# Optimization experiments

Measured on AMD Instinct MI355X. Metric: run time of the kernel, lower is better.

The kernel has to match this reference:

```python
import jax, jax.numpy as jnp
import numpy as np

B, L, HID, NH, NB = 8, 1024, 512, 8, 8
HD = HID // NH


def setup_inputs() -> dict:
    key = jax.random.key(0)
    ks = jax.random.split(key, 12)
    s = 1.0 / np.sqrt(HID)
    x = jax.random.normal(ks[0], (B, L, HID), dtype=jnp.float32)
    time_bucket_matrix = jax.random.randint(ks[1], (B, L, L), 0, NB, dtype=jnp.int32)
    causal_mask = jnp.triu(jnp.ones((L, L), dtype=bool), k=1)  # True = masked (future)
    lens = jax.random.randint(ks[2], (B,), (7 * L) // 8, L + 1)
    padding_mask = jnp.arange(L)[None, :] >= lens[:, None]  # True = pad
    return {
        "x": x,
        "time_bucket_matrix": time_bucket_matrix,
        "causal_mask": causal_mask,
        "padding_mask": padding_mask,
        "Wq": jax.random.uniform(ks[3], (HID, HID), jnp.float32, -s, s),
        "bq": jnp.zeros((HID,), jnp.float32),
        "Wk": jax.random.uniform(ks[4], (HID, HID), jnp.float32, -s, s),
        "bk": jnp.zeros((HID,), jnp.float32),
        "Wv": jax.random.uniform(ks[5], (HID, HID), jnp.float32, -s, s),
        "bv": jnp.zeros((HID,), jnp.float32),
        "Wo": jax.random.uniform(ks[6], (HID, HID), jnp.float32, -s, s),
        "bo": jnp.zeros((HID,), jnp.float32),
        "time_emb": jax.random.normal(ks[7], (NB, NH), dtype=jnp.float32),
    }


def reference(x, time_bucket_matrix, causal_mask, padding_mask,
              Wq, bq, Wk, bk, Wv, bv, Wo, bo, time_emb):
    Bb, Ll, H = x.shape
    def heads(t):
        return t.reshape(Bb, Ll, NH, HD).transpose(0, 2, 1, 3)  # [B,NH,L,HD]
    q = heads(x @ Wq.T + bq)
    k = heads(x @ Wk.T + bk)
    v = heads(x @ Wv.T + bv)
    scores = jnp.einsum("bhqd,bhkd->bhqk", q, k) / jnp.sqrt(jnp.float32(HD))
    # per-(i,j) time-bucket bias: [B,L,L] -> [B,L,L,NH] -> [B,NH,L,L]
    t_bias = time_emb[time_bucket_matrix].transpose(0, 3, 1, 2)
    scores = scores + t_bias
    scores = jnp.where(causal_mask[None, None, :, :], -1e9, scores)
    scores = jnp.where(padding_mask[:, None, None, :], -1e9, scores)  # key pad
    w = jax.nn.softmax(scores, axis=-1)
    w = jnp.where(padding_mask[:, None, :, None], 0.0, w)  # query pad
    out = jnp.einsum("bhqk,bhkd->bhqd", w, v).transpose(0, 2, 1, 3).reshape(Bb, Ll, H)
    return out @ Wo.T + bo
```

## Files before the change

kernel.cpp:

```cpp
#include <hip/hip_runtime.h>
#include <hip/hip_bf16.h>
#include <cstdint>

#define L_SEQ 1024
#define HID_DIM 512
#define N_HEADS 8
#define HEAD_DIM 64
#define BATCH 8

typedef __attribute__((ext_vector_type(8))) short bf16x8;
typedef __attribute__((ext_vector_type(4))) float f32x4;

__device__ __forceinline__ ushort f2bf(float v) {
  __hip_bfloat16 hb = __float2bfloat16(v);
  return *(ushort*)&hb;
}

__global__ __launch_bounds__(256)
void prep_convert(const float* __restrict__ x, const float* __restrict__ Wq,
                  const float* __restrict__ Wk, const float* __restrict__ Wv,
                  const float* __restrict__ Wo, ushort* __restrict__ dst) {
  const size_t gid = (size_t)blockIdx.x * 256 + threadIdx.x;
  const size_t e = gid * 8;
  const float* src;
  size_t loc;
  if (e < 4194304) {
    src = x; loc = e;
  } else {
    const size_t r = e - 4194304;
    const int wsel = (int)(r >> 18);
    loc = r & 262143;
    src = (wsel == 0) ? Wq : (wsel == 1) ? Wk : (wsel == 2) ? Wv : Wo;
  }
  float4 v0 = *(const float4*)(src + loc);
  float4 v1 = *(const float4*)(src + loc + 4);
  ushort u[8];
  u[0] = f2bf(v0.x); u[1] = f2bf(v0.y); u[2] = f2bf(v0.z); u[3] = f2bf(v0.w);
  u[4] = f2bf(v1.x); u[5] = f2bf(v1.y); u[6] = f2bf(v1.z); u[7] = f2bf(v1.w);
  *(uint4*)(dst + e) = *(uint4*)u;
}

__global__ __launch_bounds__(256)
void lens_kernel(const uint8_t* __restrict__ pm, int* __restrict__ lens) {
  __shared__ int flag;
  __shared__ int part[256];
  const int b = blockIdx.x, tid = threadIdx.x;
  if (tid == 0) flag = 0;
  __syncthreads();
  const unsigned* pw = (const unsigned*)pm;
  unsigned any = 0;
  for (int i = tid; i < 2048; i += 256) any |= (pw[i] > 1u);
  if (any) flag = 1;
  __syncthreads();
  int c = 0;
  if (flag) {
    unsigned v = pw[b * 256 + tid];
    c = (int)((v & 0xFFu) == 0) + (int)(((v >> 8) & 0xFFu) == 0) +
        (int)(((v >> 16) & 0xFFu) == 0) + (int)(((v >> 24) & 0xFFu) == 0);
  } else {
    const int* pi = (const int*)pm;
    c = (int)(pi[b * 1024 + tid * 4 + 0] == 0) + (int)(pi[b * 1024 + tid * 4 + 1] == 0) +
        (int)(pi[b * 1024 + tid * 4 + 2] == 0) + (int)(pi[b * 1024 + tid * 4 + 3] == 0);
  }
  part[tid] = c;
  __syncthreads();
  for (int s = 128; s > 0; s >>= 1) {
    if (tid < s) part[tid] += part[tid + s];
    __syncthreads();
  }
  if (tid == 0) lens[b] = part[0];
}

__global__ __launch_bounds__(256, 3)
void qkv_lds(const ushort* __restrict__ xb, const ushort* __restrict__ wqb,
             const ushort* __restrict__ wkb, const ushort* __restrict__ wvb,
             const float* __restrict__ bq, const float* __restrict__ bk,
             const float* __restrict__ bv, ushort* __restrict__ qb,
             ushort* __restrict__ kb, ushort* __restrict__ vT) {
  __shared__ char lds[2][20480];
  const int tid = threadIdx.x;
  const int w = tid >> 6, lane = tid & 63;
  const int l15 = lane & 15, g = lane >> 4;
  const int z = blockIdx.z;
  const ushort* A = (z == 2) ? wvb : xb;
  const ushort* B = (z == 0) ? wqb : (z == 1) ? wkb : xb;
  const float* bias = (z == 0) ? bq : (z == 1) ? bk : bv;
  const int M0 = ((z == 2) ? blockIdx.y : blockIdx.x) * 128;
  const int N0 = ((z == 2) ? blockIdx.x : blockIdx.y) * 128;

  const int sr = tid >> 2, sc = tid & 3;
  const ushort* Ag = A + (size_t)(M0 + sr) * 512 + sc * 8;
  const ushort* Bg = B + (size_t)(N0 + sr) * 512 + sc * 8;
  const int wro = sr * 80 + sc * 16;
  uint4 sa0, sa1, sb0, sb1;

#define QSTAGE_LOAD(kc_)                                      \
  sa0 = *(const uint4*)(Ag + (kc_) * 32);                     \
  sa1 = *(const uint4*)(Ag + (size_t)64 * 512 + (kc_) * 32);  \
  sb0 = *(const uint4*)(Bg + (kc_) * 32);                     \
  sb1 = *(const uint4*)(Bg + (size_t)64 * 512 + (kc_) * 32);
#define QSTAGE_WRITE(buf)                                     \
  *(uint4*)&(buf)[wro] = sa0;                                 \
  *(uint4*)&(buf)[wro + 64 * 80] = sa1;                       \
  *(uint4*)&(buf)[10240 + wro] = sb0;                         \
  *(uint4*)&(buf)[10240 + wro + 64 * 80] = sb1;

  const int wm = w >> 1, wn = w & 1;
  const int aro = (wm * 64 + l15) * 80 + g * 16;
  const int bro = 10240 + (wn * 64 + l15) * 80 + g * 16;

  f32x4 acc[4][4];
#pragma unroll
  for (int i = 0; i < 4; ++i)
#pragma unroll
    for (int j = 0; j < 4; ++j) acc[i][j] = (f32x4){0.f, 0.f, 0.f, 0.f};

  QSTAGE_LOAD(0);
  QSTAGE_WRITE(lds[0]);
  __syncthreads();
  int cur = 0;
#pragma unroll 1
  for (int kc = 0; kc < 16; ++kc) {
    if (kc + 1 < 16) { QSTAGE_LOAD(kc + 1); }
    bf16x8 av[4], bv[4];
#pragma unroll
    for (int t = 0; t < 4; ++t) {
      av[t] = *(const bf16x8*)&lds[cur][aro + t * 1280];
      bv[t] = *(const bf16x8*)&lds[cur][bro + t * 1280];
    }
    __builtin_amdgcn_s_setprio(1);
#pragma unroll
    for (int i = 0; i < 4; ++i)
#pragma unroll
      for (int j = 0; j < 4; ++j)
        acc[i][j] = __builtin_amdgcn_mfma_f32_16x16x32_bf16(av[i], bv[j], acc[i][j], 0, 0, 0);
    __builtin_amdgcn_s_setprio(0);
    if (kc + 1 < 16) { QSTAGE_WRITE(lds[cur ^ 1]); }
    __syncthreads();
    cur ^= 1;
  }
#undef QSTAGE_LOAD
#undef QSTAGE_WRITE

  const int M0w = M0 + wm * 64, N0w = N0 + wn * 64;
  if (z < 2) {
    ushort* out = (z == 0) ? qb : kb;
    float bn[4];
#pragma unroll
    for (int nt = 0; nt < 4; ++nt) bn[nt] = bias[N0w + nt * 16 + l15];
#pragma unroll
    for (int mt = 0; mt < 4; ++mt)
#pragma unroll
      for (int nt = 0; nt < 4; ++nt)
#pragma unroll
        for (int r = 0; r < 4; ++r) {
          const int m = M0w + mt * 16 + 4 * g + r;
          const int n = N0w + nt * 16 + l15;
          out[(size_t)m * 512 + n] = f2bf(acc[mt][nt][r] + bn[nt]);
        }
  } else {
#pragma unroll
    for (int mt = 0; mt < 4; ++mt)
#pragma unroll
      for (int r = 0; r < 4; ++r) {
        const int m = M0w + mt * 16 + 4 * g + r;
        const float bm = bias[m];
#pragma unroll
        for (int nt = 0; nt < 4; ++nt) {
          const int tok = N0w + nt * 16 + l15;
          const size_t off = ((size_t)((tok >> 10) * 512 + m)) * 1024 + (tok & 1023);
          vT[off] = f2bf(acc[mt][nt][r] + bm);
        }
      }
  }
}

__global__ __launch_bounds__(256, 3)
void out_lds(const ushort* __restrict__ A, const ushort* __restrict__ B,
             const float* __restrict__ bias, float* __restrict__ out) {
  __shared__ char lds[2][15360];
  const int tid = threadIdx.x;
  const int w = tid >> 6, lane = tid & 63;
  const int l15 = lane & 15, g = lane >> 4;
  const int M0 = blockIdx.x * 64, N0 = blockIdx.y * 128;

  const int sr = tid >> 2, sc = tid & 3;
  const ushort* Ag = A + (size_t)(M0 + sr) * 512 + sc * 8;
  const ushort* Bg = B + (size_t)(N0 + sr) * 512 + sc * 8;
  const int wro = sr * 80 + sc * 16;
  uint4 sa0, sb0, sb1;

#define OSTAGE_LOAD(kc_)                                      \
  sa0 = *(const uint4*)(Ag + (kc_) * 32);                     \
  sb0 = *(const uint4*)(Bg + (kc_) * 32);                     \
  sb1 = *(const uint4*)(Bg + (size_t)64 * 512 + (kc_) * 32);
#define OSTAGE_WRITE(buf)                                     \
  *(uint4*)&(buf)[wro] = sa0;                                 \
  *(uint4*)&(buf)[5120 + wro] = sb0;                          \
  *(uint4*)&(buf)[5120 + wro + 64 * 80] = sb1;

  const int wm = w >> 1, wn = w & 1;
  const int aro = (wm * 32 + l15) * 80 + g * 16;
  const int bro = 5120 + (wn * 64 + l15) * 80 + g * 16;

  f32x4 acc[2][4];
#pragma unroll
  for (int i = 0; i < 2; ++i)
#pragma unroll
    for (int j = 0; j < 4; ++j) acc[i][j] = (f32x4){0.f, 0.f, 0.f, 0.f};

  OSTAGE_LOAD(0);
  OSTAGE_WRITE(lds[0]);
  __syncthreads();
  int cur = 0;
#pragma unroll 1
  for (int kc = 0; kc < 16; ++kc) {
    if (kc + 1 < 16) { OSTAGE_LOAD(kc + 1); }
    bf16x8 av[2], bv[4];
#pragma unroll
    for (int t = 0; t < 2; ++t) av[t] = *(const bf16x8*)&lds[cur][aro + t * 1280];
#pragma unroll
    for (int t = 0; t < 4; ++t) bv[t] = *(const bf16x8*)&lds[cur][bro + t * 1280];
    __builtin_amdgcn_s_setprio(1);
#pragma unroll
    for (int i = 0; i < 2; ++i)
#pragma unroll
      for (int j = 0; j < 4; ++j)
        acc[i][j] = __builtin_amdgcn_mfma_f32_16x16x32_bf16(av[i], bv[j], acc[i][j], 0, 0, 0);
    __builtin_amdgcn_s_setprio(0);
    if (kc + 1 < 16) { OSTAGE_WRITE(lds[cur ^ 1]); }
    __syncthreads();
    cur ^= 1;
  }
#undef OSTAGE_LOAD
#undef OSTAGE_WRITE

  const int M0w = M0 + wm * 32, N0w = N0 + wn * 64;
  float bn[4];
#pragma unroll
  for (int nt = 0; nt < 4; ++nt) bn[nt] = bias[N0w + nt * 16 + l15];
#pragma unroll
  for (int mt = 0; mt < 2; ++mt)
#pragma unroll
    for (int nt = 0; nt < 4; ++nt)
#pragma unroll
      for (int r = 0; r < 4; ++r) {
        const int m = M0w + mt * 16 + 4 * g + r;
        const int n = N0w + nt * 16 + l15;
        out[(size_t)m * 512 + n] = acc[mt][nt][r] + bn[nt];
      }
}

__global__ __launch_bounds__(256, 2)
void attn_mfma(const ushort* __restrict__ qb, const ushort* __restrict__ kb,
               const ushort* __restrict__ vT, const int* __restrict__ tbm,
               const float* __restrict__ temb, const int* __restrict__ lens,
               ushort* __restrict__ ab) {
  __shared__ char kv[2][16384];
  __shared__ char pbuf[4][2048];
  const int tid = threadIdx.x;
  const int w = tid >> 6;
  const int lane = tid & 63;
  const int l15 = lane & 15, g = lane >> 4;
  const int b = blockIdx.x, h = blockIdx.y, p = blockIdx.z;
  const int len = lens[b];
  const int GB = 15 - p;
  const int qbaseA = p * 64 + 16 * w;
  const int qbaseB = GB * 64 + 16 * w;

  const float te_src = temb[(lane & 7) * N_HEADS + h] * 1.44269504f;

  const int r0 = tid >> 3, c0 = tid & 7;
  const size_t kgrow = (size_t)(b * L_SEQ) * HID_DIM + h * HEAD_DIM + c0 * 8;
  const size_t vgrow = (size_t)((b * 8 + h) * 64 + r0) * L_SEQ + c0 * 8;
  const int so0 = (tid * 16) ^ ((r0 & 7) << 4);
  const int so1 = so0 + 4096;
  uint4 skA, skB, svA, svB;

#define STAGE_LOAD(kc_)                                                      \
  skA = *(const uint4*)(kb + kgrow + (size_t)((kc_) + r0) * HID_DIM);        \
  skB = *(const uint4*)(kb + kgrow + (size_t)((kc_) + r0 + 32) * HID_DIM);   \
  svA = *(const uint4*)(vT + vgrow + (kc_));                                 \
  svB = *(const uint4*)(vT + vgrow + 32 * L_SEQ + (kc_));

#define STAGE_WRITE(dst)                                                     \
  *(uint4*)&(dst)[so0] = skA;                                                \
  *(uint4*)&(dst)[so1] = skB;                                                \
  *(uint4*)&(dst)[8192 + so0] = svA;                                         \
  *(uint4*)&(dst)[8192 + so1] = svB;

  bf16x8 qfA[2], qfB[2];
  {
    const ushort* qr = qb + (size_t)(b * L_SEQ + qbaseA + l15) * HID_DIM + h * HEAD_DIM + 8 * g;
    qfA[0] = *(const bf16x8*)(qr);
    qfA[1] = *(const bf16x8*)(qr + 32);
    qr = qb + (size_t)(b * L_SEQ + qbaseB + l15) * HID_DIM + h * HEAD_DIM + 8 * g;
    qfB[0] = *(const bf16x8*)(qr);
    qfB[1] = *(const bf16x8*)(qr + 32);
  }

  f32x4 OA[4], OB[4];
#pragma unroll
  for (int ct = 0; ct < 4; ++ct) {
    OA[ct] = (f32x4){0.f, 0.f, 0.f, 0.f};
    OB[ct] = (f32x4){0.f, 0.f, 0.f, 0.f};
  }
  float ssA[4] = {0.f, 0.f, 0.f, 0.f}, ssB[4] = {0.f, 0.f, 0.f, 0.f};
  bf16x8 kf[4][2], vf[2][4];
  int tbA_[4][4], tbB_[4][4];

  const int lenc = (len - 1) >> 6;
  const int nchB = (GB * 64 < len) ? ((GB < lenc ? GB : lenc) + 1) : 0;
  const int NCH = (p + 1 > nchB) ? (p + 1) : nchB;

#define LOAD_TB(dst, qbaseT, kc_)                                            \
  {                                                                          \
    const int* tb_p = tbm + (size_t)(b * L_SEQ + (qbaseT)) * L_SEQ + (kc_);  \
    _Pragma("unroll") for (int kt = 0; kt < 4; ++kt)                         \
      _Pragma("unroll") for (int r = 0; r < 4; ++r)                          \
        dst[kt][r] = tb_p[(4 * g + r) * L_SEQ + 16 * kt + l15];              \
  }

#define LOAD_KV_FRAGS(kvb)                                                   \
  _Pragma("unroll") for (int kt = 0; kt < 4; ++kt)                           \
    _Pragma("unroll") for (int db = 0; db < 2; ++db) {                       \
      const int off = ((2048 * kt + 128 * l15 + 16 * (g + 4 * db)) ^ ((l15 & 7) << 4)); \
      kf[kt][db] = *(const bf16x8*)&(kvb)[off];                              \
    }                                                                        \
  _Pragma("unroll") for (int kblk = 0; kblk < 2; ++kblk)                     \
    _Pragma("unroll") for (int ct = 0; ct < 4; ++ct) {                       \
      const int off = 8192 + ((2048 * ct + 128 * l15 + 16 * (4 * kblk + g)) ^ ((l15 & 7) << 4)); \
      vf[kblk][ct] = *(const bf16x8*)&(kvb)[off];                            \
    }

#define COMPUTE_TILE(qfv, Ov, ssumv, tbv, qbaseT, kc_)                       \
  {                                                                          \
    f32x4 s[4];                                                              \
    __builtin_amdgcn_s_setprio(1);                                           \
    _Pragma("unroll") for (int kt = 0; kt < 4; ++kt) {                       \
      s[kt] = (f32x4){0.f, 0.f, 0.f, 0.f};                                   \
      s[kt] = __builtin_amdgcn_mfma_f32_16x16x32_bf16(qfv[0], kf[kt][0], s[kt], 0, 0, 0); \
      s[kt] = __builtin_amdgcn_mfma_f32_16x16x32_bf16(qfv[1], kf[kt][1], s[kt], 0, 0, 0); \
    }                                                                        \
    __builtin_amdgcn_s_setprio(0);                                           \
    _Pragma("unroll") for (int kt = 0; kt < 4; ++kt) {                       \
      const int kg = (kc_) + 16 * kt + l15;                                  \
      _Pragma("unroll") for (int r = 0; r < 4; ++r) {                        \
        const int lr = 4 * g + r;                                            \
        const int qg = (qbaseT) + lr;                                        \
        const float te2 = __int_as_float(                                    \
            __builtin_amdgcn_ds_bpermute(tbv[kt][r] << 2, __float_as_int(te_src))); \
        float pp = exp2f(fmaf(s[kt][r], 0.18033688f, te2));                  \
        pp = (kg <= qg && qg < len) ? pp : 0.0f;                             \
        const ushort pbits = f2bf(pp);                                       \
        ssumv[r] += __bfloat162float(*(const __hip_bfloat16*)&pbits);        \
        const int off = ((lr * 128 + (16 * kt + l15) * 2) ^ ((lr & 7) << 4)); \
        *(ushort*)&pbuf[w][off] = pbits;                                     \
      }                                                                      \
    }                                                                        \
    _Pragma("unroll") for (int kblk = 0; kblk < 2; ++kblk) {                 \
      const int off = ((l15 * 128 + kblk * 64 + 16 * g) ^ ((l15 & 7) << 4)); \
      const bf16x8 pf = *(const bf16x8*)(&pbuf[w][off]);                     \
      __builtin_amdgcn_s_setprio(1);                                         \
      _Pragma("unroll") for (int ct = 0; ct < 4; ++ct)                       \
        Ov[ct] = __builtin_amdgcn_mfma_f32_16x16x32_bf16(pf, vf[kblk][ct], Ov[ct], 0, 0, 0); \
      __builtin_amdgcn_s_setprio(0);                                         \
    }                                                                        \
  }

  STAGE_LOAD(0);
  STAGE_WRITE(kv[0]);
  __syncthreads();

  int cur = 0;
  for (int c = 0; c < NCH; ++c) {
    const int kc = c * 64;
    const bool doB = (c < nchB);
    const bool doA = (c <= p);
    if (doB) LOAD_TB(tbB_, qbaseB, kc);
    if (doA) LOAD_TB(tbA_, qbaseA, kc);
    if (c + 1 < NCH) { STAGE_LOAD(kc + 64); }
    LOAD_KV_FRAGS(kv[cur]);
    if (doB) COMPUTE_TILE(qfB, OB, ssB, tbB_, qbaseB, kc);
    if (doA) COMPUTE_TILE(qfA, OA, ssA, tbA_, qbaseA, kc);
    if (c + 1 < NCH) { STAGE_WRITE(kv[cur ^ 1]); }
    __syncthreads();
    cur ^= 1;
  }

#define EPILOGUE(Ov, ssumv, qbaseT)                                          \
  {                                                                          \
    _Pragma("unroll") for (int m = 1; m <= 8; m <<= 1)                       \
      _Pragma("unroll") for (int r = 0; r < 4; ++r)                          \
        ssumv[r] += __shfl_xor(ssumv[r], m, 64);                             \
    _Pragma("unroll") for (int ct = 0; ct < 4; ++ct)                         \
      _Pragma("unroll") for (int r = 0; r < 4; ++r) {                        \
        const int qg = (qbaseT) + 4 * g + r;                                 \
        const float inv = (qg < len) ? 1.0f / ssumv[r] : 0.0f;               \
        ab[(size_t)(b * L_SEQ + qg) * HID_DIM + h * HEAD_DIM + 16 * ct + l15] = \
            f2bf(Ov[ct][r] * inv);                                           \
      }                                                                      \
  }

  EPILOGUE(OA, ssA, qbaseA);
  EPILOGUE(OB, ssB, qbaseB);
}

extern "C" void kernel_launch(void* const* d_in, const int* in_sizes, int n_in,
                              void* d_out, int out_size, void* d_ws, size_t ws_size,
                              hipStream_t stream) {
  const float* x    = (const float*)d_in[0];
  const int*   tbm  = (const int*)d_in[1];
  const uint8_t* pm = (const uint8_t*)d_in[3];
  const float* Wq = (const float*)d_in[4];
  const float* bq = (const float*)d_in[5];
  const float* Wk = (const float*)d_in[6];
  const float* bk = (const float*)d_in[7];
  const float* Wv = (const float*)d_in[8];
  const float* bv = (const float*)d_in[9];
  const float* Wo = (const float*)d_in[10];
  const float* bo = (const float*)d_in[11];
  const float* temb = (const float*)d_in[12];
  float* out = (float*)d_out;

  const size_t NTOK = (size_t)BATCH * L_SEQ * HID_DIM;
  const size_t NW = 262144;
  ushort* ab  = (ushort*)d_ws;
  ushort* xb  = ab + NTOK;
  ushort* wqb = xb + NTOK;
  ushort* wkb = wqb + NW;
  ushort* wvb = wkb + NW;
  ushort* wob = wvb + NW;
  ushort* qb  = wob + NW;
  ushort* kb  = qb + NTOK;
  ushort* vT  = kb + NTOK;
  int* lens   = (int*)(vT + NTOK);

  prep_convert<<<2560, 256, 0, stream>>>(x, Wq, Wk, Wv, Wo, xb);
  lens_kernel<<<8, 256, 0, stream>>>(pm, lens);
  qkv_lds<<<dim3(64, 4, 3), 256, 0, stream>>>(xb, wqb, wkb, wvb, bq, bk, bv, qb, kb, vT);
  attn_mfma<<<dim3(8, 8, 8), 256, 0, stream>>>(qb, kb, vT, tbm, temb, lens, ab);
  out_lds<<<dim3(128, 4), 256, 0, stream>>>(ab, wob, bo, out);
}
```

Before: 84.97 us.

## Split paired causal query tiles into separate blocks with higher occupancy

```diff
diff --git a/kernel.cpp b/kernel.cpp
--- a/kernel.cpp
+++ b/kernel.cpp
@@ -251,7 +251,7 @@
       }
 }
 
-__global__ __launch_bounds__(256, 2)
+__global__ __launch_bounds__(256, 4)
 void attn_mfma(const ushort* __restrict__ qb, const ushort* __restrict__ kb,
                const ushort* __restrict__ vT, const int* __restrict__ tbm,
                const float* __restrict__ temb, const int* __restrict__ lens,
@@ -262,11 +262,10 @@
   const int w = tid >> 6;
   const int lane = tid & 63;
   const int l15 = lane & 15, g = lane >> 4;
-  const int b = blockIdx.x, h = blockIdx.y, p = blockIdx.z;
+  const int b = blockIdx.x, h = blockIdx.y;
+  const int qg = 15 - blockIdx.z;
   const int len = lens[b];
-  const int GB = 15 - p;
-  const int qbaseA = p * 64 + 16 * w;
-  const int qbaseB = GB * 64 + 16 * w;
+  const int qbase = qg * 64 + 16 * w;
 
   const float te_src = temb[(lane & 7) * N_HEADS + h] * 1.44269504f;
 
@@ -289,121 +288,116 @@
   *(uint4*)&(dst)[8192 + so0] = svA;                                         \
   *(uint4*)&(dst)[8192 + so1] = svB;
 
-  bf16x8 qfA[2], qfB[2];
+  bf16x8 qf[2];
   {
-    const ushort* qr = qb + (size_t)(b * L_SEQ + qbaseA + l15) * HID_DIM + h * HEAD_DIM + 8 * g;
-    qfA[0] = *(const bf16x8*)(qr);
-    qfA[1] = *(const bf16x8*)(qr + 32);
-    qr = qb + (size_t)(b * L_SEQ + qbaseB + l15) * HID_DIM + h * HEAD_DIM + 8 * g;
-    qfB[0] = *(const bf16x8*)(qr);
-    qfB[1] = *(const bf16x8*)(qr + 32);
-  }
-
-  f32x4 OA[4], OB[4];
-#pragma unroll
-  for (int ct = 0; ct < 4; ++ct) {
-    OA[ct] = (f32x4){0.f, 0.f, 0.f, 0.f};
-    OB[ct] = (f32x4){0.f, 0.f, 0.f, 0.f};
-  }
-  float ssA[4] = {0.f, 0.f, 0.f, 0.f}, ssB[4] = {0.f, 0.f, 0.f, 0.f};
-  bf16x8 kf[4][2], vf[2][4];
-  int tbA_[4][4], tbB_[4][4];
+    const ushort* qr = qb + (size_t)(b * L_SEQ + qbase + l15) * HID_DIM + h * HEAD_DIM + 8 * g;
+    qf[0] = *(const bf16x8*)(qr);
+    qf[1] = *(const bf16x8*)(qr + 32);
+  }
+
+  f32x4 O[4];
+#pragma unroll
+  for (int ct = 0; ct < 4; ++ct) O[ct] = (f32x4){0.f, 0.f, 0.f, 0.f};
+  float ssum[4] = {0.f, 0.f, 0.f, 0.f};
+  int tb_[4][4];
 
   const int lenc = (len - 1) >> 6;
-  const int nchB = (GB * 64 < len) ? ((GB < lenc ? GB : lenc) + 1) : 0;
-  const int NCH = (p + 1 > nchB) ? (p + 1) : nchB;
-
-#define LOAD_TB(dst, qbaseT, kc_)                                            \
-  {                                                                          \
-    const int* tb_p = tbm + (size_t)(b * L_SEQ + (qbaseT)) * L_SEQ + (kc_);  \
-    _Pragma("unroll") for (int kt = 0; kt < 4; ++kt)                         \
-      _Pragma("unroll") for (int r = 0; r < 4; ++r)                          \
-        dst[kt][r] = tb_p[(4 * g + r) * L_SEQ + 16 * kt + l15];              \
-  }
-
-#define LOAD_KV_FRAGS(kvb)                                                   \
-  _Pragma("unroll") for (int kt = 0; kt < 4; ++kt)                           \
-    _Pragma("unroll") for (int db = 0; db < 2; ++db) {                       \
-      const int off = ((2048 * kt + 128 * l15 + 16 * (g + 4 * db)) ^ ((l15 & 7) << 4)); \
-      kf[kt][db] = *(const bf16x8*)&(kvb)[off];                              \
-    }                                                                        \
-  _Pragma("unroll") for (int kblk = 0; kblk < 2; ++kblk)                     \
-    _Pragma("unroll") for (int ct = 0; ct < 4; ++ct) {                       \
-      const int off = 8192 + ((2048 * ct + 128 * l15 + 16 * (4 * kblk + g)) ^ ((l15 & 7) << 4)); \
-      vf[kblk][ct] = *(const bf16x8*)&(kvb)[off];                            \
+  const int nch = (qg * 64 < len) ? ((qg < lenc ? qg : lenc) + 1) : 0;
+  const int* tbq = tbm + (size_t)(b * L_SEQ + qbase) * L_SEQ;
+
+  if (nch > 0) {
+    STAGE_LOAD(0);
+    STAGE_WRITE(kv[0]);
+  }
+  __syncthreads();
+
+  int cur = 0;
+#pragma unroll 1
+  for (int c = 0; c < nch; ++c) {
+    const int kc = c * 64;
+#pragma unroll
+    for (int kt = 0; kt < 4; ++kt)
+#pragma unroll
+      for (int r = 0; r < 4; ++r)
+        tb_[kt][r] = tbq[(size_t)(4 * g + r) * L_SEQ + kc + 16 * kt + l15];
+    if (c + 1 < nch) { STAGE_LOAD(kc + 64); }
+
+    bf16x8 kf[4][2];
+#pragma unroll
+    for (int kt = 0; kt < 4; ++kt)
+#pragma unroll
+      for (int db = 0; db < 2; ++db) {
+        const int off = ((2048 * kt + 128 * l15 + 16 * (g + 4 * db)) ^ ((l15 & 7) << 4));
+        kf[kt][db] = *(const bf16x8*)&kv[cur][off];
+      }
+    f32x4 s[4];
+    __builtin_amdgcn_s_setprio(1);
+#pragma unroll
+    for (int kt = 0; kt < 4; ++kt) {
+      s[kt] = (f32x4){0.f, 0.f, 0.f, 0.f};
+      s[kt] = __builtin_amdgcn_mfma_f32_16x16x32_bf16(qf[0], kf[kt][0], s[kt], 0, 0, 0);
+      s[kt] = __builtin_amdgcn_mfma_f32_16x16x32_bf16(qf[1], kf[kt][1], s[kt], 0, 0, 0);
     }
-
-#define COMPUTE_TILE(qfv, Ov, ssumv, tbv, qbaseT, kc_)                       \
-  {                                                                          \
-    f32x4 s[4];                                                              \
-    __builtin_amdgcn_s_setprio(1);                                           \
-    _Pragma("unroll") for (int kt = 0; kt < 4; ++kt) {                       \
-      s[kt] = (f32x4){0.f, 0.f, 0.f, 0.f};                                   \
-      s[kt] = __builtin_amdgcn_mfma_f32_16x16x32_bf16(qfv[0], kf[kt][0], s[kt], 0, 0, 0); \
-      s[kt] = __builtin_amdgcn_mfma_f32_16x16x32_bf16(qfv[1], kf[kt][1], s[kt], 0, 0, 0); \
-    }                                                                        \
-    __builtin_amdgcn_s_setprio(0);                                           \
-    _Pragma("unroll") for (int kt = 0; kt < 4; ++kt) {                       \
-      const int kg = (kc_) + 16 * kt + l15;                                  \
-      _Pragma("unroll") for (int r = 0; r < 4; ++r) {                        \
-        const int lr = 4 * g + r;                                            \
-        const int qg = (qbaseT) + lr;                                        \
-        const float te2 = __int_as_float(                                    \
-            __builtin_amdgcn_ds_bpermute(tbv[kt][r] << 2, __float_as_int(te_src))); \
-        float pp = exp2f(fmaf(s[kt][r], 0.18033688f, te2));                  \
-        pp = (kg <= qg && qg < len) ? pp : 0.0f;                             \
-        const ushort pbits = f2bf(pp);                                       \
-        ssumv[r] += __bfloat162float(*(const __hip_bfloat16*)&pbits);        \
-        const int off = ((lr * 128 + (16 * kt + l15) * 2) ^ ((lr & 7) << 4)); \
-        *(ushort*)&pbuf[w][off] = pbits;                                     \
-      }                                                                      \
-    }                                                                        \
-    _Pragma("unroll") for (int kblk = 0; kblk < 2; ++kblk) {                 \
-      const int off = ((l15 * 128 + kblk * 64 + 16 * g) ^ ((l15 & 7) << 4)); \
-      const bf16x8 pf = *(const bf16x8*)(&pbuf[w][off]);                     \
-      __builtin_amdgcn_s_setprio(1);                                         \
-      _Pragma("unroll") for (int ct = 0; ct < 4; ++ct)                       \
-        Ov[ct] = __builtin_amdgcn_mfma_f32_16x16x32_bf16(pf, vf[kblk][ct], Ov[ct], 0, 0, 0); \
-      __builtin_amdgcn_s_setprio(0);                                         \
-    }                                                                        \
-  }
-
-  STAGE_LOAD(0);
-  STAGE_WRITE(kv[0]);
-  __syncthreads();
-
-  int cur = 0;
-  for (int c = 0; c < NCH; ++c) {
-    const int kc = c * 64;
-    const bool doB = (c < nchB);
-    const bool doA = (c <= p);
-    if (doB) LOAD_TB(tbB_, qbaseB, kc);
-    if (doA) LOAD_TB(tbA_, qbaseA, kc);
-    if (c + 1 < NCH) { STAGE_LOAD(kc + 64); }
-    LOAD_KV_FRAGS(kv[cur]);
-    if (doB) COMPUTE_TILE(qfB, OB, ssB, tbB_, qbaseB, kc);
-    if (doA) COMPUTE_TILE(qfA, OA, ssA, tbA_, qbaseA, kc);
-    if (c + 1 < NCH) { STAGE_WRITE(kv[cur ^ 1]); }
+    __builtin_amdgcn_s_setprio(0);
+
+    bf16x8 vf[2][4];
+#pragma unroll
+    for (int kblk = 0; kblk < 2; ++kblk)
+#pragma unroll
+      for (int ct = 0; ct < 4; ++ct) {
+        const int off = 8192 + ((2048 * ct + 128 * l15 + 16 * (4 * kblk + g)) ^ ((l15 & 7) << 4));
+        vf[kblk][ct] = *(const bf16x8*)&kv[cur][off];
+      }
+
+#pragma unroll
+    for (int kt = 0; kt < 4; ++kt) {
+      const int kg = kc + 16 * kt + l15;
+#pragma unroll
+      for (int r = 0; r < 4; ++r) {
+        const int lr = 4 * g + r;
+        const int qgr = qbase + lr;
+        const float te2 = __int_as_float(
+            __builtin_amdgcn_ds_bpermute(tb_[kt][r] << 2, __float_as_int(te_src)));
+        float pp = exp2f(fmaf(s[kt][r], 0.18033688f, te2));
+        pp = (kg <= qgr && qgr < len) ? pp : 0.0f;
+        ssum[r] += pp;
+        const int off = ((lr * 128 + (16 * kt + l15) * 2) ^ ((lr & 7) << 4));
+        *(ushort*)&pbuf[w][off] = f2bf(pp);
+      }
+    }
+
+#pragma unroll
+    for (int kblk = 0; kblk < 2; ++kblk) {
+      const int off = ((l15 * 128 + kblk * 64 + 16 * g) ^ ((l15 & 7) << 4));
+      const bf16x8 pf = *(const bf16x8*)(&pbuf[w][off]);
+      __builtin_amdgcn_s_setprio(1);
+#pragma unroll
+      for (int ct = 0; ct < 4; ++ct)
+        O[ct] = __builtin_amdgcn_mfma_f32_16x16x32_bf16(pf, vf[kblk][ct], O[ct], 0, 0, 0);
+      __builtin_amdgcn_s_setprio(0);
+    }
+
+    if (c + 1 < nch) { STAGE_WRITE(kv[cur ^ 1]); }
     __syncthreads();
     cur ^= 1;
   }
-
-#define EPILOGUE(Ov, ssumv, qbaseT)                                          \
-  {                                                                          \
-    _Pragma("unroll") for (int m = 1; m <= 8; m <<= 1)                       \
-      _Pragma("unroll") for (int r = 0; r < 4; ++r)                          \
-        ssumv[r] += __shfl_xor(ssumv[r], m, 64);                             \
-    _Pragma("unroll") for (int ct = 0; ct < 4; ++ct)                         \
-      _Pragma("unroll") for (int r = 0; r < 4; ++r) {                        \
-        const int qg = (qbaseT) + 4 * g + r;                                 \
-        const float inv = (qg < len) ? 1.0f / ssumv[r] : 0.0f;               \
-        ab[(size_t)(b * L_SEQ + qg) * HID_DIM + h * HEAD_DIM + 16 * ct + l15] = \
-            f2bf(Ov[ct][r] * inv);                                           \
-      }                                                                      \
-  }
-
-  EPILOGUE(OA, ssA, qbaseA);
-  EPILOGUE(OB, ssB, qbaseB);
+#undef STAGE_LOAD
+#undef STAGE_WRITE
+
+#pragma unroll
+  for (int m = 1; m <= 8; m <<= 1) {
+#pragma unroll
+    for (int r = 0; r < 4; ++r) ssum[r] += __shfl_xor(ssum[r], m, 64);
+  }
+#pragma unroll
+  for (int ct = 0; ct < 4; ++ct)
+#pragma unroll
+    for (int r = 0; r < 4; ++r) {
+      const int qgr = qbase + 4 * g + r;
+      const float inv = (qgr < len && nch > 0) ? 1.0f / ssum[r] : 0.0f;
+      ab[(size_t)(b * L_SEQ + qgr) * HID_DIM + h * HEAD_DIM + 16 * ct + l15] =
+          f2bf(O[ct][r] * inv);
+    }
 }
 
 extern "C" void kernel_launch(void* const* d_in, const int* in_sizes, int n_in,
@@ -439,6 +433,6 @@
   prep_convert<<<2560, 256, 0, stream>>>(x, Wq, Wk, Wv, Wo, xb);
   lens_kernel<<<8, 256, 0, stream>>>(pm, lens);
   qkv_lds<<<dim3(64, 4, 3), 256, 0, stream>>>(xb, wqb, wkb, wvb, bq, bk, bv, qb, kb, vT);
-  attn_mfma<<<dim3(8, 8, 8), 256, 0, stream>>>(qb, kb, vT, tbm, temb, lens, ab);
+  attn_mfma<<<dim3(8, 8, 16), 256, 0, stream>>>(qb, kb, vT, tbm, temb, lens, ab);
   out_lds<<<dim3(128, 4), 256, 0, stream>>>(ab, wob, bo, out);
 }
```

After: 126.2 us. 48.5% more time.
